# Kernel tuning notes

Hardware: AMD Instinct MI355X
Metric: run time of the kernel (lower is better)

## Reference

```python
import jax, jax.numpy as jnp
import numpy as np

D_MODEL = 512
D_FFN = 4 * D_MODEL
EPS = 1e-5


def layer_norm(x, gamma, beta):
    mu = jnp.mean(x, axis=-1, keepdims=True)
    var = jnp.mean(jnp.square(x - mu), axis=-1, keepdims=True)
    return (x - mu) * jax.lax.rsqrt(var + EPS) * gamma + beta


def setup_inputs() -> dict:
    key = jax.random.key(0)
    ks = jax.random.split(key, 12)
    B, S, D, F = 4, 2048, D_MODEL, D_FFN
    s = 1.0 / np.sqrt(D)
    inp = {
        "q": jax.random.normal(ks[0], (B, S, D), jnp.float32),
        "k": jax.random.normal(ks[1], (B, S, D), jnp.float32),
        "v": jax.random.normal(ks[2], (B, S, D), jnp.float32),
        "x": jax.random.normal(ks[3], (B, S, D), jnp.float32),
        "Wq": jax.random.normal(ks[4], (D, D), jnp.float32) * s,
        "bq": jnp.zeros((D,), jnp.float32),
        "Wk": jax.random.normal(ks[5], (D, D), jnp.float32) * s,
        "bk": jnp.zeros((D,), jnp.float32),
        "Wv": jax.random.normal(ks[6], (D, D), jnp.float32) * s,
        "bv": jnp.zeros((D,), jnp.float32),
        "g1": jnp.ones((D,), jnp.float32),
        "be1": jnp.zeros((D,), jnp.float32),
        "W1": jax.random.normal(ks[7], (D, F), jnp.float32) * s,
        "b1": jnp.zeros((F,), jnp.float32),
        "W2": jax.random.normal(ks[8], (F, D), jnp.float32) * (1.0 / np.sqrt(F)),
        "b2": jnp.zeros((D,), jnp.float32),
        "g2": jnp.ones((D,), jnp.float32),
        "be2": jnp.zeros((D,), jnp.float32),
    }
    return inp


def reference(q, k, v, x, Wq, bq, Wk, bk, Wv, bv, g1, be1, W1, b1, W2, b2, g2, be2):
    # QKV projections: [B,S,D] @ [D,D]
    Q = jnp.einsum("bsd,de->bse", q, Wq) + bq
    K = jnp.einsum("bsd,de->bse", k, Wk) + bk
    V = jnp.einsum("bsd,de->bse", v, Wv) + bv
    d_k = Q.shape[-1]
    # scaled dot-product attention, full [B,S,S] scores as in the original
    scores = jnp.einsum("bqd,bkd->bqk", Q, K) / jnp.sqrt(jnp.float32(d_k))
    probs = jax.nn.softmax(scores, axis=-1)
    attn = jnp.einsum("bqk,bkd->bqd", probs, V)
    # residual + LayerNorm
    h = layer_norm(attn + x, g1, be1)
    # position-wise FFN
    f = jnp.maximum(jnp.einsum("bsd,df->bsf", h, W1) + b1, 0.0)
    f = jnp.einsum("bsf,fd->bsd", f, W2) + b2
    # residual + LayerNorm
    return layer_norm(f + h, g2, be2)
```

## Files before the change

kernel.cpp:

```cpp
#include <hip/hip_runtime.h>


typedef __attribute__((ext_vector_type(8))) short short8;
typedef __attribute__((ext_vector_type(4))) float f32x4;

#define BARRIER()   asm volatile("s_barrier" ::: "memory")
#define WAITVM(N)   asm volatile("s_waitcnt vmcnt(" #N ")" ::: "memory")
#define WAITLGKM0() asm volatile("s_waitcnt lgkmcnt(0)" ::: "memory")

__device__ __forceinline__ unsigned short f2bf(float f) {
    unsigned int u = __float_as_uint(f);
    unsigned int r = (u + 0x7FFFu + ((u >> 16) & 1u)) >> 16;
    return (unsigned short)r;
}

__device__ __forceinline__ void gload_lds16(const void* g, void* l) {
    __builtin_amdgcn_global_load_lds(
        (const __attribute__((address_space(1))) void*)g,
        (__attribute__((address_space(3))) void*)l, 16, 0, 0);
}

__global__ __launch_bounds__(256) void cast_f32_bf16(
    const float* __restrict__ in, unsigned short* __restrict__ out, long n4) {
    long i = (long)blockIdx.x * blockDim.x + threadIdx.x;
    if (i < n4) {
        float4 v = ((const float4*)in)[i];
        ushort4 o;
        o.x = f2bf(v.x); o.y = f2bf(v.y); o.z = f2bf(v.z); o.w = f2bf(v.w);
        ((ushort4*)out)[i] = o;
    }
}

__global__ __launch_bounds__(256) void concat3(
    const float* __restrict__ a, const float* __restrict__ b,
    const float* __restrict__ c, float* __restrict__ o, int n) {
    int i = blockIdx.x * blockDim.x + threadIdx.x;
    if (i < n) o[i] = a[i];
    else if (i < 2 * n) o[i] = b[i - n];
    else if (i < 3 * n) o[i] = c[i - 2 * n];
}

__global__ __launch_bounds__(256) void transpose_cast_f32_bf16(
    const float* __restrict__ in, unsigned short* __restrict__ out, int R, int C) {
    __shared__ float t[32][33];
    int c0 = blockIdx.x * 32, r0 = blockIdx.y * 32;
    int x = threadIdx.x;
    for (int i = threadIdx.y; i < 32; i += 8)
        t[i][x] = in[(long)(r0 + i) * C + c0 + x];
    __syncthreads();
    for (int i = threadIdx.y; i < 32; i += 8)
        out[(long)(c0 + i) * R + r0 + x] = f2bf(t[x][i]);
}

__global__ __launch_bounds__(256) void transpose_bf16(
    const unsigned short* __restrict__ in, unsigned short* __restrict__ out,
    int R, int C, int inLd, long inBatch, long outBatch) {
    __shared__ unsigned short t[32][33];
    long z = blockIdx.z;
    in += z * inBatch; out += z * outBatch;
    int c0 = blockIdx.x * 32, r0 = blockIdx.y * 32;
    int x = threadIdx.x;
    for (int i = threadIdx.y; i < 32; i += 8)
        t[i][x] = in[(long)(r0 + i) * inLd + c0 + x];
    __syncthreads();
    for (int i = threadIdx.y; i < 32; i += 8)
        out[(long)(c0 + i) * R + r0 + x] = t[x][i];
}

template<int BIAS, int RELU, int OUT_BF16>
__global__ __launch_bounds__(512, 2) void gemm256(
    const unsigned short* __restrict__ A, const unsigned short* __restrict__ BT,
    const float* __restrict__ bias, void* __restrict__ C,
    int K, int lda, int ldb, int ldc,
    long aBatch, long bBatch, long cBatch,
    long aKOff, long bKOff, long cKOff, int zDiv,
    long aGroup, float scale) {
    __shared__ __align__(16) unsigned short As[2][16384];
    __shared__ __align__(16) unsigned short Bs[2][16384];
    const int tid  = threadIdx.x;
    const int wave = tid >> 6;
    const int lane = tid & 63;
    const int wm = wave >> 2;
    const int wn = wave & 3;
    const int z = blockIdx.z;
    const int b = z / zDiv;
    const int kc = z - b * zDiv;
    const int row0 = blockIdx.y * 256;
    const int col0 = blockIdx.x * 256;
    A  += (long)b * aBatch + (long)kc * aKOff + (long)(col0 >> 9) * aGroup
        + (long)row0 * lda;
    BT += (long)b * bBatch + (long)kc * bKOff + (long)col0 * ldb;
    const long cOff = (long)b * cBatch + (long)kc * cKOff;

    f32x4 acc[8][4] = {};

    const int sr = tid >> 3;
    const int sc = (tid & 7) ^ (sr & 7);
    const long aSrcOff = (long)sr * lda + sc * 8;
    const long bSrcOff = (long)sr * ldb + sc * 8;
    const int ldst = wave << 9;
    const int nt = K >> 6;

    const int rA = lane & 15, l4 = lane >> 4;
    const int cp0 = ((l4)     ^ (rA & 7)) << 3;
    const int cp1 = ((4 + l4) ^ (rA & 7)) << 3;

#define STAGE_A(t, a) gload_lds16(A  + (long)(t) * 64 + (long)(a) * 64 * lda + aSrcOff, \
                                  &As[(t) & 1][(a) * 4096 + ldst])
#define STAGE_B(t, a) gload_lds16(BT + (long)(t) * 64 + (long)(a) * 64 * ldb + bSrcOff, \
                                  &Bs[(t) & 1][(a) * 4096 + ldst])

    STAGE_B(0, 0); STAGE_B(0, 1); STAGE_B(0, 2); STAGE_B(0, 3);
    STAGE_A(0, 0); STAGE_A(0, 1); STAGE_A(0, 2); STAGE_A(0, 3);
    STAGE_B(1, 0); STAGE_B(1, 1); STAGE_B(1, 2); STAGE_B(1, 3);
    STAGE_A(1, 0); STAGE_A(1, 2);
    WAITVM(6);
    BARRIER();

    for (int t = 0; t < nt; ++t) {
        const int buf = t & 1;
        short8 bfr[4][2];
        short8 afr[2][2];
        #pragma unroll
        for (int fn = 0; fn < 4; ++fn) {
            const int rb = (wn * 64 + fn * 16 + rA) * 64;
            bfr[fn][0] = *(const short8*)&Bs[buf][rb + cp0];
            bfr[fn][1] = *(const short8*)&Bs[buf][rb + cp1];
        }
        #pragma unroll
        for (int i = 0; i < 2; ++i) {
            const int ra = (wm * 128 + i * 16 + rA) * 64;
            afr[i][0] = *(const short8*)&As[buf][ra + cp0];
            afr[i][1] = *(const short8*)&As[buf][ra + cp1];
        }
        if (t + 1 < nt) { STAGE_A(t + 1, 1); STAGE_A(t + 1, 3); }
        BARRIER();
        WAITLGKM0();
        __builtin_amdgcn_sched_barrier(0);
        __builtin_amdgcn_s_setprio(1);
        #pragma unroll
        for (int ks = 0; ks < 2; ++ks)
            #pragma unroll
            for (int i = 0; i < 2; ++i)
                #pragma unroll
                for (int fn = 0; fn < 4; ++fn)
                    acc[i][fn] = __builtin_amdgcn_mfma_f32_16x16x32_bf16(
                        afr[i][ks], bfr[fn][ks], acc[i][fn], 0, 0, 0);
        __builtin_amdgcn_s_setprio(0);
        BARRIER();
        #pragma unroll
        for (int q = 1; q < 4; ++q) {
            #pragma unroll
            for (int i = 0; i < 2; ++i) {
                const int ra = (wm * 128 + (2 * q + i) * 16 + rA) * 64;
                afr[i][0] = *(const short8*)&As[buf][ra + cp0];
                afr[i][1] = *(const short8*)&As[buf][ra + cp1];
            }
            if (q == 1 && t + 2 < nt) { STAGE_B(t + 2, 0); STAGE_B(t + 2, 1); }
            if (q == 2 && t + 2 < nt) { STAGE_B(t + 2, 2); STAGE_B(t + 2, 3); }
            if (q == 3 && t + 2 < nt) { STAGE_A(t + 2, 0); STAGE_A(t + 2, 2); }
            BARRIER();
            WAITLGKM0();
            __builtin_amdgcn_sched_barrier(0);
            __builtin_amdgcn_s_setprio(1);
            #pragma unroll
            for (int ks = 0; ks < 2; ++ks)
                #pragma unroll
                for (int i = 0; i < 2; ++i)
                    #pragma unroll
                    for (int fn = 0; fn < 4; ++fn)
                        acc[2 * q + i][fn] = __builtin_amdgcn_mfma_f32_16x16x32_bf16(
                            afr[i][ks], bfr[fn][ks], acc[2 * q + i][fn], 0, 0, 0);
            __builtin_amdgcn_s_setprio(0);
            if (q == 1 && t == nt - 1) { WAITVM(0); }
            if (q == 3) {
                if (t + 2 < nt)       { WAITVM(6); }
                else if (t + 2 == nt) { WAITVM(2); }
            }
            BARRIER();
        }
    }
#undef STAGE_A
#undef STAGE_B

    const int orow = row0 + wm * 128 + l4 * 4;
    const int ocol = col0 + wn * 64 + rA;
    #pragma unroll
    for (int fn = 0; fn < 4; ++fn) {
        const int cc = ocol + fn * 16;
        float bv = 0.0f;
        if (BIAS) bv = bias[cc];
        #pragma unroll
        for (int fm = 0; fm < 8; ++fm) {
            #pragma unroll
            for (int j = 0; j < 4; ++j) {
                float v = acc[fm][fn][j] * scale + bv;
                if (RELU) v = fmaxf(v, 0.0f);
                long off = cOff + (long)(orow + fm * 16 + j) * ldc + cc;
                if (OUT_BF16) ((unsigned short*)C)[off] = f2bf(v);
                else          ((float*)C)[off] = v;
            }
        }
    }
}

__global__ __launch_bounds__(256) void softmax_rows(
    const float* __restrict__ S, unsigned short* __restrict__ P) {
    long row = blockIdx.x;
    const float4* src = (const float4*)(S + row * 2048);
    int tid = threadIdx.x;
    int wave = tid >> 6, lane = tid & 63;
    float4 a = src[tid], b = src[tid + 256];
    float e[8] = { a.x, a.y, a.z, a.w, b.x, b.y, b.z, b.w };
    float m = e[0];
    #pragma unroll
    for (int i = 1; i < 8; ++i) m = fmaxf(m, e[i]);
    #pragma unroll
    for (int o = 32; o > 0; o >>= 1) m = fmaxf(m, __shfl_xor(m, o));
    __shared__ float redm[4], reds[4];
    if (lane == 0) redm[wave] = m;
    __syncthreads();
    m = fmaxf(fmaxf(redm[0], redm[1]), fmaxf(redm[2], redm[3]));
    float s = 0.0f;
    #pragma unroll
    for (int i = 0; i < 8; ++i) { e[i] = __expf(e[i] - m); s += e[i]; }
    #pragma unroll
    for (int o = 32; o > 0; o >>= 1) s += __shfl_xor(s, o);
    if (lane == 0) reds[wave] = s;
    __syncthreads();
    s = reds[0] + reds[1] + reds[2] + reds[3];
    float inv = 1.0f / s;
    ushort4 o0, o1;
    o0.x = f2bf(e[0] * inv); o0.y = f2bf(e[1] * inv);
    o0.z = f2bf(e[2] * inv); o0.w = f2bf(e[3] * inv);
    o1.x = f2bf(e[4] * inv); o1.y = f2bf(e[5] * inv);
    o1.z = f2bf(e[6] * inv); o1.w = f2bf(e[7] * inv);
    ushort4* dst = (ushort4*)(P + row * 2048);
    dst[tid] = o0;
    dst[tid + 256] = o1;
}

template<int NPART, int BIASF, int DUAL>
__global__ __launch_bounds__(128) void ln_kernel(
    const float* __restrict__ A0, long partOff, const float* __restrict__ R,
    const float* __restrict__ bias,
    const float* __restrict__ g, const float* __restrict__ be,
    float* __restrict__ out, unsigned short* __restrict__ outbf) {
    long row = blockIdx.x;
    int tid = threadIdx.x;
    int wave = tid >> 6, lane = tid & 63;
    float4 v = ((const float4*)(R + row * 512))[tid];
    #pragma unroll
    for (int p = 0; p < NPART; ++p) {
        float4 vp = ((const float4*)(A0 + p * partOff + row * 512))[tid];
        v.x += vp.x; v.y += vp.y; v.z += vp.z; v.w += vp.w;
    }
    if (BIASF) {
        float4 vb = ((const float4*)bias)[tid];
        v.x += vb.x; v.y += vb.y; v.z += vb.z; v.w += vb.w;
    }
    float s  = v.x + v.y + v.z + v.w;
    float s2 = v.x * v.x + v.y * v.y + v.z * v.z + v.w * v.w;
    #pragma unroll
    for (int o = 32; o > 0; o >>= 1) { s += __shfl_xor(s, o); s2 += __shfl_xor(s2, o); }
    __shared__ float r1[2], r2[2];
    if (lane == 0) { r1[wave] = s; r2[wave] = s2; }
    __syncthreads();
    s = r1[0] + r1[1]; s2 = r2[0] + r2[1];
    float mu = s * (1.0f / 512.0f);
    float var = s2 * (1.0f / 512.0f) - mu * mu;
    float rs = rsqrtf(var + 1e-5f);
    float4 gg = ((const float4*)g)[tid];
    float4 bb = ((const float4*)be)[tid];
    float4 y;
    y.x = (v.x - mu) * rs * gg.x + bb.x;
    y.y = (v.y - mu) * rs * gg.y + bb.y;
    y.z = (v.z - mu) * rs * gg.z + bb.z;
    y.w = (v.w - mu) * rs * gg.w + bb.w;
    ((float4*)(out + row * 512))[tid] = y;
    if (DUAL) {
        ushort4 o;
        o.x = f2bf(y.x); o.y = f2bf(y.y); o.z = f2bf(y.z); o.w = f2bf(y.w);
        ((ushort4*)(outbf + row * 512))[tid] = o;
    }
}

extern "C" void kernel_launch(void* const* d_in, const int* in_sizes, int n_in,
                              void* d_out, int out_size, void* d_ws, size_t ws_size,
                              hipStream_t stream) {
    const float* q   = (const float*)d_in[0];
    const float* k   = (const float*)d_in[1];
    const float* v   = (const float*)d_in[2];
    const float* x   = (const float*)d_in[3];
    const float* Wq  = (const float*)d_in[4];
    const float* bq  = (const float*)d_in[5];
    const float* Wk  = (const float*)d_in[6];
    const float* bk  = (const float*)d_in[7];
    const float* Wv  = (const float*)d_in[8];
    const float* bv  = (const float*)d_in[9];
    const float* g1  = (const float*)d_in[10];
    const float* be1 = (const float*)d_in[11];
    const float* W1  = (const float*)d_in[12];
    const float* b1  = (const float*)d_in[13];
    const float* W2  = (const float*)d_in[14];
    const float* b2  = (const float*)d_in[15];
    const float* g2  = (const float*)d_in[16];
    const float* be2 = (const float*)d_in[17];
    float* out = (float*)d_out;

    const int B = 4, S = 2048, D = 512, F = 2048;
    const long BS = (long)B * S;
    const long SD = (long)S * D;
    const long SS = (long)S * S;
    const int N3 = 3 * D;

    char* ws = (char*)d_ws;
    size_t off = 0;
    auto alloc = [&](size_t bytes) -> void* {
        void* p = ws + off;
        off += (bytes + 255) & ~(size_t)255;
        return p;
    };
    unsigned short* WqkvT = (unsigned short*)alloc((size_t)N3 * D * 2);
    unsigned short* W1T   = (unsigned short*)alloc((size_t)D * F * 2);
    unsigned short* W2T   = (unsigned short*)alloc((size_t)F * D * 2);
    float* bqkv           = (float*)alloc((size_t)N3 * 4);
    unsigned short* qkv_in = (unsigned short*)alloc(3 * BS * D * 2);
    unsigned short* VT = qkv_in;
    unsigned short* QKV = (unsigned short*)alloc(BS * (size_t)N3 * 2);
    float* h_f32 = (float*)QKV;
    unsigned short* h_bf = (unsigned short*)((char*)QKV + BS * D * 4);
    float* Sc = (float*)alloc((size_t)B * SS * 4);
    float* attnP = Sc;
    float* f2P   = Sc;
    unsigned short* Pb = (unsigned short*)alloc((size_t)B * SS * 2);
    unsigned short* f_bf = Pb;

    const float scale = 0.04419417382415922f;

    {
        long n4 = BS * D / 4;
        int blocks = (int)((n4 + 255) / 256);
        cast_f32_bf16<<<blocks, 256, 0, stream>>>(q, qkv_in, n4);
        cast_f32_bf16<<<blocks, 256, 0, stream>>>(k, qkv_in + BS * D, n4);
        cast_f32_bf16<<<blocks, 256, 0, stream>>>(v, qkv_in + 2 * BS * D, n4);
    }
    transpose_cast_f32_bf16<<<dim3(D/32, D/32), dim3(32, 8), 0, stream>>>(Wq, WqkvT, D, D);
    transpose_cast_f32_bf16<<<dim3(D/32, D/32), dim3(32, 8), 0, stream>>>(Wk, WqkvT + (size_t)D * D, D, D);
    transpose_cast_f32_bf16<<<dim3(D/32, D/32), dim3(32, 8), 0, stream>>>(Wv, WqkvT + 2 * (size_t)D * D, D, D);
    transpose_cast_f32_bf16<<<dim3(F/32, D/32), dim3(32, 8), 0, stream>>>(W1, W1T, D, F);
    transpose_cast_f32_bf16<<<dim3(D/32, F/32), dim3(32, 8), 0, stream>>>(W2, W2T, F, D);
    concat3<<<(3 * D + 255) / 256, 256, 0, stream>>>(bq, bk, bv, bqkv, D);
    gemm256<1,0,1><<<dim3(N3/256, 32, 1), 512, 0, stream>>>(
        qkv_in, WqkvT, bqkv, QKV, D, D, D, N3,
        0, 0, 0, 0, 0, 0, 1, BS * D, 1.0f);
    transpose_bf16<<<dim3(D/32, S/32, B), dim3(32, 8), 0, stream>>>(
        QKV + 2 * D, VT, S, D, N3, (long)S * N3, SD);
    gemm256<0,0,0><<<dim3(S/256, S/256, B), 512, 0, stream>>>(
        QKV, QKV + D, nullptr, Sc, D, N3, N3, S,
        (long)S * N3, (long)S * N3, SS, 0, 0, 0, 1, 0, scale);
    softmax_rows<<<(int)BS, 256, 0, stream>>>(Sc, Pb);
    gemm256<0,0,0><<<dim3(D/256, S/256, 4 * B), 512, 0, stream>>>(
        Pb, VT, nullptr, attnP, S / 4, S, S, D,
        SS, SD, SD, S / 4, S / 4, BS * D, 4, 0, 1.0f);
    ln_kernel<4,0,1><<<(int)BS, 128, 0, stream>>>(attnP, BS * D, x, nullptr, g1, be1, h_f32, h_bf);
    gemm256<1,1,1><<<dim3(F/256, 32, 1), 512, 0, stream>>>(
        h_bf, W1T, b1, f_bf, D, D, D, F,
        0, 0, 0, 0, 0, 0, 1, 0, 1.0f);
    gemm256<0,0,0><<<dim3(D/256, 32, 4), 512, 0, stream>>>(
        f_bf, W2T, nullptr, f2P, F / 4, F, F, D,
        0, 0, 0, F / 4, F / 4, BS * D, 4, 0, 1.0f);
    ln_kernel<4,1,0><<<(int)BS, 128, 0, stream>>>(f2P, BS * D, h_f32, b2, g2, be2, out, nullptr);
}
```

Measured before the change: 364.9 us.

## Fuse prep kernels, store scores in bf16, replace split-K GEMMs with smaller-tile GEMM

The three input casts become one launch, and all weight transposes plus the bias concat become a single prep launch. The QKV GEMM now writes V transposed directly from its epilogue, so the separate transpose kernel goes away. Attention scores are stored as bf16 instead of fp32, which halves softmax traffic at some cost in precision. The split-K P·V and FFN2 GEMMs, which needed partial-sum reduction in LayerNorm, are replaced by a new 128x64-tile non-split GEMM, and LayerNorm now reads a single partial.

```diff
diff --git a/kernel.cpp b/kernel.cpp
--- a/kernel.cpp
+++ b/kernel.cpp
@@ -13,6 +13,9 @@
     unsigned int r = (u + 0x7FFFu + ((u >> 16) & 1u)) >> 16;
     return (unsigned short)r;
 }
+__device__ __forceinline__ float bf2f(unsigned short u) {
+    return __uint_as_float((unsigned int)u << 16);
+}
 
 __device__ __forceinline__ void gload_lds16(const void* g, void* l) {
     __builtin_amdgcn_global_load_lds(
@@ -20,30 +23,53 @@
         (__attribute__((address_space(3))) void*)l, 16, 0, 0);
 }
 
-__global__ __launch_bounds__(256) void cast_f32_bf16(
-    const float* __restrict__ in, unsigned short* __restrict__ out, long n4) {
+__global__ __launch_bounds__(256) void cast3_f32_bf16(
+    const float* __restrict__ q, const float* __restrict__ k,
+    const float* __restrict__ v, unsigned short* __restrict__ out, long n4) {
     long i = (long)blockIdx.x * blockDim.x + threadIdx.x;
-    if (i < n4) {
-        float4 v = ((const float4*)in)[i];
-        ushort4 o;
-        o.x = f2bf(v.x); o.y = f2bf(v.y); o.z = f2bf(v.z); o.w = f2bf(v.w);
-        ((ushort4*)out)[i] = o;
-    }
-}
-
-__global__ __launch_bounds__(256) void concat3(
-    const float* __restrict__ a, const float* __restrict__ b,
-    const float* __restrict__ c, float* __restrict__ o, int n) {
-    int i = blockIdx.x * blockDim.x + threadIdx.x;
-    if (i < n) o[i] = a[i];
-    else if (i < 2 * n) o[i] = b[i - n];
-    else if (i < 3 * n) o[i] = c[i - 2 * n];
-}
-
-__global__ __launch_bounds__(256) void transpose_cast_f32_bf16(
-    const float* __restrict__ in, unsigned short* __restrict__ out, int R, int C) {
+    if (i >= 3 * n4) return;
+    const float* src; long j;
+    if (i < n4)          { src = q; j = i; }
+    else if (i < 2 * n4) { src = k; j = i - n4; }
+    else                 { src = v; j = i - 2 * n4; }
+    float4 vv = ((const float4*)src)[j];
+    ushort4 o;
+    o.x = f2bf(vv.x); o.y = f2bf(vv.y); o.z = f2bf(vv.z); o.w = f2bf(vv.w);
+    ((ushort4*)out)[i] = o;
+}
+
+__global__ __launch_bounds__(256) void prep_weights(
+    const float* __restrict__ Wq, const float* __restrict__ Wk,
+    const float* __restrict__ Wv, const float* __restrict__ W1,
+    const float* __restrict__ W2,
+    const float* __restrict__ bq, const float* __restrict__ bk,
+    const float* __restrict__ bv,
+    unsigned short* __restrict__ WqkvT, unsigned short* __restrict__ W1T,
+    unsigned short* __restrict__ W2T, float* __restrict__ bqkv) {
+    int z = blockIdx.x;
+    if (z >= 2816) {
+        int i = (z - 2816) * 256 + threadIdx.y * 32 + threadIdx.x;
+        float val = (i < 512) ? bq[i] : (i < 1024) ? bk[i - 512] : bv[i - 1024];
+        bqkv[i] = val;
+        return;
+    }
     __shared__ float t[32][33];
-    int c0 = blockIdx.x * 32, r0 = blockIdx.y * 32;
+    const float* in; unsigned short* out; int R, C, r0, c0;
+    if (z < 768) {
+        int w = z >> 8, zz = z & 255;
+        in = (w == 0) ? Wq : (w == 1) ? Wk : Wv;
+        out = WqkvT + (size_t)w * 512 * 512;
+        R = 512; C = 512;
+        c0 = (zz & 15) * 32; r0 = (zz >> 4) * 32;
+    } else if (z < 1792) {
+        int zz = z - 768;
+        in = W1; out = W1T; R = 512; C = 2048;
+        c0 = (zz & 63) * 32; r0 = (zz >> 6) * 32;
+    } else {
+        int zz = z - 1792;
+        in = W2; out = W2T; R = 2048; C = 512;
+        c0 = (zz & 15) * 32; r0 = (zz >> 4) * 32;
+    }
     int x = threadIdx.x;
     for (int i = threadIdx.y; i < 32; i += 8)
         t[i][x] = in[(long)(r0 + i) * C + c0 + x];
@@ -52,29 +78,14 @@
         out[(long)(c0 + i) * R + r0 + x] = f2bf(t[x][i]);
 }
 
-__global__ __launch_bounds__(256) void transpose_bf16(
-    const unsigned short* __restrict__ in, unsigned short* __restrict__ out,
-    int R, int C, int inLd, long inBatch, long outBatch) {
-    __shared__ unsigned short t[32][33];
-    long z = blockIdx.z;
-    in += z * inBatch; out += z * outBatch;
-    int c0 = blockIdx.x * 32, r0 = blockIdx.y * 32;
-    int x = threadIdx.x;
-    for (int i = threadIdx.y; i < 32; i += 8)
-        t[i][x] = in[(long)(r0 + i) * inLd + c0 + x];
-    __syncthreads();
-    for (int i = threadIdx.y; i < 32; i += 8)
-        out[(long)(c0 + i) * R + r0 + x] = t[x][i];
-}
-
-template<int BIAS, int RELU, int OUT_BF16>
+template<int BIAS, int RELU, int OUT_BF16, int VTROPT>
 __global__ __launch_bounds__(512, 2) void gemm256(
     const unsigned short* __restrict__ A, const unsigned short* __restrict__ BT,
     const float* __restrict__ bias, void* __restrict__ C,
     int K, int lda, int ldb, int ldc,
     long aBatch, long bBatch, long cBatch,
-    long aKOff, long bKOff, long cKOff, int zDiv,
-    long aGroup, float scale) {
+    long aGroup, float scale,
+    unsigned short* __restrict__ VT, int vS, long vBatch) {
     __shared__ __align__(16) unsigned short As[2][16384];
     __shared__ __align__(16) unsigned short Bs[2][16384];
     const int tid  = threadIdx.x;
@@ -82,15 +93,12 @@
     const int lane = tid & 63;
     const int wm = wave >> 2;
     const int wn = wave & 3;
-    const int z = blockIdx.z;
-    const int b = z / zDiv;
-    const int kc = z - b * zDiv;
+    const int b = blockIdx.z;
     const int row0 = blockIdx.y * 256;
     const int col0 = blockIdx.x * 256;
-    A  += (long)b * aBatch + (long)kc * aKOff + (long)(col0 >> 9) * aGroup
-        + (long)row0 * lda;
-    BT += (long)b * bBatch + (long)kc * bKOff + (long)col0 * ldb;
-    const long cOff = (long)b * cBatch + (long)kc * cKOff;
+    A  += (long)b * aBatch + (long)(col0 >> 9) * aGroup + (long)row0 * lda;
+    BT += (long)b * bBatch + (long)col0 * ldb;
+    const long cOff = (long)b * cBatch;
 
     f32x4 acc[8][4] = {};
 
@@ -185,6 +193,26 @@
 
     const int orow = row0 + wm * 128 + l4 * 4;
     const int ocol = col0 + wn * 64 + rA;
+    if (VTROPT && col0 >= 1024) {
+        const int bb = orow >> 11, s0 = orow & 2047;
+        #pragma unroll
+        for (int fn = 0; fn < 4; ++fn) {
+            const int cc = ocol + fn * 16;
+            const int d = cc - 1024;
+            float bv = 0.0f;
+            if (BIAS) bv = bias[cc];
+            #pragma unroll
+            for (int fm = 0; fm < 8; ++fm) {
+                ushort4 o;
+                o.x = f2bf(acc[fm][fn][0] * scale + bv);
+                o.y = f2bf(acc[fm][fn][1] * scale + bv);
+                o.z = f2bf(acc[fm][fn][2] * scale + bv);
+                o.w = f2bf(acc[fm][fn][3] * scale + bv);
+                *(ushort4*)(VT + (long)bb * vBatch + (long)d * vS + s0 + fm * 16) = o;
+            }
+        }
+        return;
+    }
     #pragma unroll
     for (int fn = 0; fn < 4; ++fn) {
         const int cc = ocol + fn * 16;
@@ -204,14 +232,103 @@
     }
 }
 
+template<int BN, int BIAS, int RELU, int OUT_BF16>
+__global__ __launch_bounds__(256, 2) void gemm_nt(
+    const unsigned short* __restrict__ A, const unsigned short* __restrict__ BT,
+    const float* __restrict__ bias, void* __restrict__ C,
+    int K, int lda, int ldb, int ldc,
+    long aBatch, long bBatch, long cBatch, float scale) {
+    constexpr int NF = BN / 32;
+    __shared__ __align__(16) unsigned short As[2][4096];
+    __shared__ __align__(16) unsigned short Bs[2][BN * 32];
+    const int tid  = threadIdx.x;
+    const int wave = tid >> 6;
+    const int lane = tid & 63;
+    const int z = blockIdx.z;
+    A  += (long)z * aBatch;
+    BT += (long)z * bBatch;
+    const int row0 = blockIdx.y * 128;
+    const int col0 = blockIdx.x * BN;
+    const int wr = (wave >> 1) * 64;
+    const int wc = (wave & 1) * (BN / 2);
+
+    f32x4 acc[4][NF] = {};
+
+    const int fs = ((tid >> 2) & 3) ^ ((tid >> 4) & 3);
+    const unsigned short* Ag = A  + (long)(row0 + (tid >> 2)) * lda + (((tid & 3) ^ fs) << 3);
+    const unsigned short* Bg = BT + (long)(col0 + (tid >> 2)) * ldb + (((tid & 3) ^ fs) << 3);
+    const int sBase = wave * 512;
+
+    const int lr  = lane & 15;
+    const int fr  = (lr & 3) ^ ((lr >> 2) & 3);
+    const int kq8 = (((lane >> 4) ^ fr) << 3);
+    const int nk = K >> 5;
+
+    #pragma unroll
+    for (int c = 0; c < 2; ++c)
+        gload_lds16(Ag + (long)c * 64 * lda, &As[0][sBase + c * 2048]);
+    #pragma unroll
+    for (int c = 0; c < BN / 64; ++c)
+        gload_lds16(Bg + (long)c * 64 * ldb, &Bs[0][sBase + c * 2048]);
+    __syncthreads();
+
+    for (int t = 0; t < nk; ++t) {
+        const int cur = t & 1;
+        if (t + 1 < nk) {
+            const int k0 = (t + 1) << 5;
+            #pragma unroll
+            for (int c = 0; c < 2; ++c)
+                gload_lds16(Ag + (long)c * 64 * lda + k0, &As[cur ^ 1][sBase + c * 2048]);
+            #pragma unroll
+            for (int c = 0; c < BN / 64; ++c)
+                gload_lds16(Bg + (long)c * 64 * ldb + k0, &Bs[cur ^ 1][sBase + c * 2048]);
+        }
+        short8 af[4], bf[NF];
+        #pragma unroll
+        for (int m = 0; m < 4; ++m)
+            af[m] = *(const short8*)&As[cur][(wr + m * 16 + lr) * 32 + kq8];
+        #pragma unroll
+        for (int n = 0; n < NF; ++n)
+            bf[n] = *(const short8*)&Bs[cur][(wc + n * 16 + lr) * 32 + kq8];
+        #pragma unroll
+        for (int m = 0; m < 4; ++m)
+            #pragma unroll
+            for (int n = 0; n < NF; ++n)
+                acc[m][n] = __builtin_amdgcn_mfma_f32_16x16x32_bf16(
+                    af[m], bf[n], acc[m][n], 0, 0, 0);
+        __syncthreads();
+    }
+
+    const int orow = row0 + wr + (lane >> 4) * 4;
+    const int ocol = col0 + wc + lr;
+    #pragma unroll
+    for (int n = 0; n < NF; ++n) {
+        const int cc = ocol + n * 16;
+        float bv = 0.0f;
+        if (BIAS) bv = bias[cc];
+        #pragma unroll
+        for (int m = 0; m < 4; ++m) {
+            #pragma unroll
+            for (int j = 0; j < 4; ++j) {
+                float v = acc[m][n][j] * scale + bv;
+                if (RELU) v = fmaxf(v, 0.0f);
+                long off = (long)z * cBatch + (long)(orow + m * 16 + j) * ldc + cc;
+                if (OUT_BF16) ((unsigned short*)C)[off] = f2bf(v);
+                else          ((float*)C)[off] = v;
+            }
+        }
+    }
+}
+
 __global__ __launch_bounds__(256) void softmax_rows(
-    const float* __restrict__ S, unsigned short* __restrict__ P) {
+    const unsigned short* __restrict__ S, unsigned short* __restrict__ P) {
     long row = blockIdx.x;
-    const float4* src = (const float4*)(S + row * 2048);
     int tid = threadIdx.x;
     int wave = tid >> 6, lane = tid & 63;
-    float4 a = src[tid], b = src[tid + 256];
-    float e[8] = { a.x, a.y, a.z, a.w, b.x, b.y, b.z, b.w };
+    short8 a = ((const short8*)(S + row * 2048))[tid];
+    float e[8];
+    #pragma unroll
+    for (int i = 0; i < 8; ++i) e[i] = bf2f((unsigned short)a[i]);
     float m = e[0];
     #pragma unroll
     for (int i = 1; i < 8; ++i) m = fmaxf(m, e[i]);
@@ -230,35 +347,24 @@
     __syncthreads();
     s = reds[0] + reds[1] + reds[2] + reds[3];
     float inv = 1.0f / s;
-    ushort4 o0, o1;
-    o0.x = f2bf(e[0] * inv); o0.y = f2bf(e[1] * inv);
-    o0.z = f2bf(e[2] * inv); o0.w = f2bf(e[3] * inv);
-    o1.x = f2bf(e[4] * inv); o1.y = f2bf(e[5] * inv);
-    o1.z = f2bf(e[6] * inv); o1.w = f2bf(e[7] * inv);
-    ushort4* dst = (ushort4*)(P + row * 2048);
-    dst[tid] = o0;
-    dst[tid + 256] = o1;
-}
-
-template<int NPART, int BIASF, int DUAL>
+    short8 o;
+    #pragma unroll
+    for (int i = 0; i < 8; ++i) o[i] = (short)f2bf(e[i] * inv);
+    ((short8*)(P + row * 2048))[tid] = o;
+}
+
+template<int DUAL>
 __global__ __launch_bounds__(128) void ln_kernel(
-    const float* __restrict__ A0, long partOff, const float* __restrict__ R,
-    const float* __restrict__ bias,
+    const float* __restrict__ A0, const float* __restrict__ R,
     const float* __restrict__ g, const float* __restrict__ be,
     float* __restrict__ out, unsigned short* __restrict__ outbf) {
     long row = blockIdx.x;
     int tid = threadIdx.x;
     int wave = tid >> 6, lane = tid & 63;
-    float4 v = ((const float4*)(R + row * 512))[tid];
-    #pragma unroll
-    for (int p = 0; p < NPART; ++p) {
-        float4 vp = ((const float4*)(A0 + p * partOff + row * 512))[tid];
-        v.x += vp.x; v.y += vp.y; v.z += vp.z; v.w += vp.w;
-    }
-    if (BIASF) {
-        float4 vb = ((const float4*)bias)[tid];
-        v.x += vb.x; v.y += vb.y; v.z += vb.z; v.w += vb.w;
-    }
+    float4 va = ((const float4*)(A0 + row * 512))[tid];
+    float4 vr = ((const float4*)(R + row * 512))[tid];
+    float4 v;
+    v.x = va.x + vr.x; v.y = va.y + vr.y; v.z = va.z + vr.z; v.w = va.w + vr.w;
     float s  = v.x + v.y + v.z + v.w;
     float s2 = v.x * v.x + v.y * v.y + v.z * v.z + v.w * v.w;
     #pragma unroll
@@ -326,49 +432,39 @@
     unsigned short* W2T   = (unsigned short*)alloc((size_t)F * D * 2);
     float* bqkv           = (float*)alloc((size_t)N3 * 4);
     unsigned short* qkv_in = (unsigned short*)alloc(3 * BS * D * 2);
-    unsigned short* VT = qkv_in;
+    float* attn = (float*)qkv_in;
     unsigned short* QKV = (unsigned short*)alloc(BS * (size_t)N3 * 2);
     float* h_f32 = (float*)QKV;
     unsigned short* h_bf = (unsigned short*)((char*)QKV + BS * D * 4);
-    float* Sc = (float*)alloc((size_t)B * SS * 4);
-    float* attnP = Sc;
-    float* f2P   = Sc;
+    unsigned short* VT = (unsigned short*)alloc(BS * D * 2);
+    unsigned short* Sc = (unsigned short*)alloc((size_t)B * SS * 2);
+    unsigned short* f_bf = Sc;
     unsigned short* Pb = (unsigned short*)alloc((size_t)B * SS * 2);
-    unsigned short* f_bf = Pb;
+    float* f2 = (float*)Pb;
 
     const float scale = 0.04419417382415922f;
 
     {
         long n4 = BS * D / 4;
-        int blocks = (int)((n4 + 255) / 256);
-        cast_f32_bf16<<<blocks, 256, 0, stream>>>(q, qkv_in, n4);
-        cast_f32_bf16<<<blocks, 256, 0, stream>>>(k, qkv_in + BS * D, n4);
-        cast_f32_bf16<<<blocks, 256, 0, stream>>>(v, qkv_in + 2 * BS * D, n4);
-    }
-    transpose_cast_f32_bf16<<<dim3(D/32, D/32), dim3(32, 8), 0, stream>>>(Wq, WqkvT, D, D);
-    transpose_cast_f32_bf16<<<dim3(D/32, D/32), dim3(32, 8), 0, stream>>>(Wk, WqkvT + (size_t)D * D, D, D);
-    transpose_cast_f32_bf16<<<dim3(D/32, D/32), dim3(32, 8), 0, stream>>>(Wv, WqkvT + 2 * (size_t)D * D, D, D);
-    transpose_cast_f32_bf16<<<dim3(F/32, D/32), dim3(32, 8), 0, stream>>>(W1, W1T, D, F);
-    transpose_cast_f32_bf16<<<dim3(D/32, F/32), dim3(32, 8), 0, stream>>>(W2, W2T, F, D);
-    concat3<<<(3 * D + 255) / 256, 256, 0, stream>>>(bq, bk, bv, bqkv, D);
-    gemm256<1,0,1><<<dim3(N3/256, 32, 1), 512, 0, stream>>>(
+        cast3_f32_bf16<<<(int)((3 * n4 + 255) / 256), 256, 0, stream>>>(
+            q, k, v, qkv_in, n4);
+    }
+    prep_weights<<<2822, dim3(32, 8), 0, stream>>>(
+        Wq, Wk, Wv, W1, W2, bq, bk, bv, WqkvT, W1T, W2T, bqkv);
+    gemm256<1,0,1,1><<<dim3(N3/256, 32, 1), 512, 0, stream>>>(
         qkv_in, WqkvT, bqkv, QKV, D, D, D, N3,
-        0, 0, 0, 0, 0, 0, 1, BS * D, 1.0f);
-    transpose_bf16<<<dim3(D/32, S/32, B), dim3(32, 8), 0, stream>>>(
-        QKV + 2 * D, VT, S, D, N3, (long)S * N3, SD);
-    gemm256<0,0,0><<<dim3(S/256, S/256, B), 512, 0, stream>>>(
+        0, 0, 0, BS * D, 1.0f, VT, S, SD);
+    gemm256<0,0,1,0><<<dim3(S/256, S/256, B), 512, 0, stream>>>(
         QKV, QKV + D, nullptr, Sc, D, N3, N3, S,
-        (long)S * N3, (long)S * N3, SS, 0, 0, 0, 1, 0, scale);
+        (long)S * N3, (long)S * N3, SS, 0, scale, nullptr, 0, 0);
     softmax_rows<<<(int)BS, 256, 0, stream>>>(Sc, Pb);
-    gemm256<0,0,0><<<dim3(D/256, S/256, 4 * B), 512, 0, stream>>>(
-        Pb, VT, nullptr, attnP, S / 4, S, S, D,
-        SS, SD, SD, S / 4, S / 4, BS * D, 4, 0, 1.0f);
-    ln_kernel<4,0,1><<<(int)BS, 128, 0, stream>>>(attnP, BS * D, x, nullptr, g1, be1, h_f32, h_bf);
-    gemm256<1,1,1><<<dim3(F/256, 32, 1), 512, 0, stream>>>(
+    gemm_nt<64,0,0,0><<<dim3(D/64, S/128, B), 256, 0, stream>>>(
+        Pb, VT, nullptr, attn, S, S, S, D, SS, SD, SD, 1.0f);
+    ln_kernel<1><<<(int)BS, 128, 0, stream>>>(attn, x, g1, be1, h_f32, h_bf);
+    gemm256<1,1,1,0><<<dim3(F/256, 32, 1), 512, 0, stream>>>(
         h_bf, W1T, b1, f_bf, D, D, D, F,
-        0, 0, 0, 0, 0, 0, 1, 0, 1.0f);
-    gemm256<0,0,0><<<dim3(D/256, 32, 4), 512, 0, stream>>>(
-        f_bf, W2T, nullptr, f2P, F / 4, F, F, D,
-        0, 0, 0, F / 4, F / 4, BS * D, 4, 0, 1.0f);
-    ln_kernel<4,1,0><<<(int)BS, 128, 0, stream>>>(f2P, BS * D, h_f32, b2, g2, be2, out, nullptr);
-}
+        0, 0, 0, 0, 1.0f, nullptr, 0, 0);
+    gemm_nt<64,1,0,0><<<dim3(D/64, (int)BS/128, 1), 256, 0, stream>>>(
+        f_bf, W2T, b2, f2, F, F, F, D, 0, 0, 0, 1.0f);
+    ln_kernel<0><<<(int)BS, 128, 0, stream>>>(f2, h_f32, g2, be2, out, nullptr);
+}
```

After: 349.4 us. 1.04x faster.
